# Kernel optimization log

Hardware: AMD Instinct MI355X
Metric: run time of the kernel (lower is better)

## Reference

```python
import jax, jax.numpy as jnp
import numpy as np

WINDOW_SIZE = 11
CHANNEL = 3
PAD = WINDOW_SIZE // 2
C1 = 0.01 ** 2
C2 = 0.03 ** 2
LEVEL_WEIGHTS = np.array([0.0448, 0.2856, 0.3001, 0.2363, 0.1333], dtype=np.float32)


def _make_window():
    # 1D Gaussian, sigma=1.5, normalized; outer product -> 2D window
    x = np.arange(WINDOW_SIZE, dtype=np.float32)
    g = np.exp(-((x - WINDOW_SIZE // 2) ** 2) / (2.0 * 1.5 ** 2))
    g = g / g.sum()
    w2 = np.outer(g, g).astype(np.float32)  # [11,11]
    # depthwise kernel [C, 1, 11, 11]
    return jnp.asarray(np.tile(w2[None, None], (CHANNEL, 1, 1, 1)))


def setup_inputs() -> dict:
    key = jax.random.key(0)
    k1, k2 = jax.random.split(key)
    img1 = jax.random.uniform(k1, (16, 3, 512, 512), dtype=jnp.float32)
    # correlated second image so cs stays positive (cs**weight well-defined)
    img2 = jnp.clip(img1 + 0.05 * jax.random.normal(k2, img1.shape, dtype=jnp.float32), 0.0, 1.0)
    return {"img1": img1, "img2": img2, "window": _make_window()}


def _dwconv(x, window):
    # depthwise 11x11 conv, SAME padding (pad=5), groups=C
    return jax.lax.conv_general_dilated(
        x, window, window_strides=(1, 1), padding=[(PAD, PAD), (PAD, PAD)],
        feature_group_count=CHANNEL,
        dimension_numbers=("NCHW", "OIHW", "NCHW"))


def _ssim_and_cs(img1, img2, window):
    mu1 = _dwconv(img1, window)
    mu2 = _dwconv(img2, window)
    mu1_sq = mu1 * mu1
    mu2_sq = mu2 * mu2
    mu1_mu2 = mu1 * mu2
    sigma1_sq = _dwconv(img1 * img1, window) - mu1_sq
    sigma2_sq = _dwconv(img2 * img2, window) - mu2_sq
    sigma12 = _dwconv(img1 * img2, window) - mu1_mu2
    cs_map = (2.0 * sigma12 + C2) / (sigma1_sq + sigma2_sq + C2)
    ssim_map = (2.0 * mu1_mu2 + C1) / (mu1_sq + mu2_sq + C1) * cs_map
    return jnp.mean(ssim_map), jnp.mean(cs_map)


def _avg_pool2(x):
    B, C, H, W = x.shape
    return x.reshape(B, C, H // 2, 2, W // 2, 2).mean(axis=(3, 5))


def reference(img1, img2, window):
    weights = jnp.asarray(LEVEL_WEIGHTS)
    levels = weights.shape[0]
    mssim, mcs = [], []
    for i in range(levels):
        s, c = _ssim_and_cs(img1, img2, window)
        mssim.append(s)
        mcs.append(c)
        if i < levels - 1:
            img1 = _avg_pool2(img1)
            img2 = _avg_pool2(img2)
    mssim = jnp.stack(mssim)
    mcs = jnp.stack(mcs)
    return jnp.prod(mcs[:-1] ** weights[:-1]) * mssim[-1] ** weights[-1]
```

## Files before the change

### kernel.cpp

```cpp
#include <hip/hip_runtime.h>
#include <math.h>

#define TW 16
#define THT 64
#define HRT 74
#define SS 66
#define HS 64
#define SC1 0.0001f
#define SC2 0.0009f
#define PLANES 48
#define NSLOT 64

typedef float v2f __attribute__((ext_vector_type(2)));

struct alignas(16) Smem {
    float sb[HRT * SS];
    float hb[HRT * HS];
    float rbuf[8];
};

__device__ __forceinline__ void ssim_tile(
        Smem* sm,
        const float* __restrict__ p1, const float* __restrict__ p2,
        int H, int W, int tx, int ty, int level,
        const float* __restrict__ window,
        float* __restrict__ accum,
        float* __restrict__ l1a, float* __restrict__ l1b,
        float* __restrict__ l2a, float* __restrict__ l2b,
        float* __restrict__ l3a, float* __restrict__ l3b,
        float* __restrict__ l4a, float* __restrict__ l4b)
{
    const int tid = threadIdx.x;
    float* sb = sm->sb;
    float* hb = sm->hb;

    float g[11];
    {
        float invg5 = 1.0f / sqrtf(window[60]);
        #pragma unroll
        for (int k = 0; k < 11; ++k) g[k] = window[55 + k] * invg5;
    }

    const bool interior = (ty >= 5) && (ty + HRT - 6 < H) &&
                          (tx >= 8) && (tx + 24 <= W);
    if (interior) {
        for (int s = tid; s < HRT * 8; s += 256) {
            int r = s >> 3, j = s & 7;
            size_t o = (size_t)(ty + r - 5) * W + (tx - 8 + 4 * j);
            float4 a = *(const float4*)(p1 + o);
            float4 b = *(const float4*)(p2 + o);
            float* d = &sb[SS * r + 8 * j];
            *(float2*)(d)     = make_float2(a.x + b.x, a.x - b.x);
            *(float2*)(d + 2) = make_float2(a.y + b.y, a.y - b.y);
            *(float2*)(d + 4) = make_float2(a.z + b.z, a.z - b.z);
            *(float2*)(d + 6) = make_float2(a.w + b.w, a.w - b.w);
        }
    } else {
        for (int s = tid; s < HRT * 16; s += 256) {
            int r = s >> 4, j = s & 15;
            int gy = ty + r - 5;
            int gx = tx - 8 + 2 * j;
            float2 v1 = make_float2(0.f, 0.f), v2 = make_float2(0.f, 0.f);
            if ((unsigned)gy < (unsigned)H && (unsigned)gx < (unsigned)W) {
                size_t o = (size_t)gy * W + gx;
                v1 = *(const float2*)(p1 + o);
                v2 = *(const float2*)(p2 + o);
            }
            float* d = &sb[SS * r + 4 * j];
            *(float2*)(d)     = make_float2(v1.x + v2.x, v1.x - v2.x);
            *(float2*)(d + 2) = make_float2(v1.y + v2.y, v1.y - v2.y);
        }
    }
    __syncthreads();

    if (l1a) {
        int pc = tid & 7;
        int pr = tid >> 3;
        int r  = 2 * pr + 5;
        int x0 = 2 * (2 * pc + 8);
        const v2f* r0p = (const v2f*)&sb[SS * r + x0];
        const v2f* r1p = (const v2f*)&sb[SS * (r + 1) + x0];
        v2f s = (r0p[0] + r0p[1]) + (r1p[0] + r1p[1]);
        int W2 = W >> 1;
        size_t o = (size_t)((ty >> 1) + pr) * W2 + (tx >> 1) + pc;
        l1a[o] = 0.125f * (s.x + s.y);
        l1b[o] = 0.125f * (s.x - s.y);
    }

    if (l1a && tid >= 192) {
        const int lane = tid - 192;
        int qr = lane >> 2, qc = lane & 3;
        int rb = 4 * qr + 5, cb = 4 * qc + 8;
        v2f acc = {0.f, 0.f};
        #pragma unroll
        for (int i = 0; i < 4; ++i) {
            int ii = (i + qc) & 3;
            #pragma unroll
            for (int j = 0; j < 4; ++j) {
                int jr = (j + qr) & 3;
                acc += *(const v2f*)&sb[SS * (rb + ii) + 2 * (cb + jr)];
            }
        }
        float v2a = 0.03125f * (acc.x + acc.y), v2b = 0.03125f * (acc.x - acc.y);
        {
            int W4 = W >> 2;
            size_t o = (size_t)((ty >> 2) + qr) * W4 + (tx >> 2) + qc;
            l2a[o] = v2a;
            l2b[o] = v2b;
        }
        float v3a, v3b;
        {
            int tr = (lane >> 1) & 7, tc = lane & 1;
            int l00 = 8 * tr + 2 * tc;
            v3a = 0.25f * (__shfl(v2a, l00) + __shfl(v2a, l00 + 1) +
                           __shfl(v2a, l00 + 4) + __shfl(v2a, l00 + 5));
            v3b = 0.25f * (__shfl(v2b, l00) + __shfl(v2b, l00 + 1) +
                           __shfl(v2b, l00 + 4) + __shfl(v2b, l00 + 5));
            if (lane < 16) {
                int W8 = W >> 3;
                size_t o = (size_t)((ty >> 3) + tr) * W8 + (tx >> 3) + tc;
                l3a[o] = v3a;
                l3b[o] = v3b;
            }
        }
        {
            int ur = lane & 3;
            float v4a = 0.25f * (__shfl(v3a, 4 * ur) + __shfl(v3a, 4 * ur + 1) +
                                 __shfl(v3a, 4 * ur + 2) + __shfl(v3a, 4 * ur + 3));
            float v4b = 0.25f * (__shfl(v3b, 4 * ur) + __shfl(v3b, 4 * ur + 1) +
                                 __shfl(v3b, 4 * ur + 2) + __shfl(v3b, 4 * ur + 3));
            if (lane < 4) {
                int W16 = W >> 4;
                size_t o = (size_t)((ty >> 4) + ur) * W16 + (tx >> 4);
                l4a[o] = v4a;
                l4b[o] = v4b;
            }
        }
    }

    for (int gi = tid; gi < HRT * 8; gi += 256) {
        int r  = gi >> 3;
        int c0 = (gi & 7) << 1;
        const v2f* src = (const v2f*)&sb[SS * r + 2 * (c0 + 3)];
        v2f am_a = {0,0}, aq_a = {0,0};
        v2f am_b = {0,0}, aq_b = {0,0};
        #pragma unroll
        for (int k = 0; k < 12; ++k) {
            v2f uv = src[k];
            v2f sq = uv * uv;
            if (k < 11) {
                v2f gg = {g[k], g[k]};
                am_a += gg * uv;
                aq_a += gg * sq;
            }
            if (k >= 1) {
                v2f gg = {g[k - 1], g[k - 1]};
                am_b += gg * uv;
                aq_b += gg * sq;
            }
        }
        int rx = (r & 1) << 2;
        *(float4*)&hb[HS * r + ((4 * c0)     ^ rx)] = make_float4(am_a.x, am_a.y, aq_a.x, aq_a.y);
        *(float4*)&hb[HS * r + ((4 * c0 + 4) ^ rx)] = make_float4(am_b.x, am_b.y, aq_b.x, aq_b.y);
    }
    __syncthreads();

    float ssum = 0.f, csum = 0.f;
    {
        int c  = tid & 15;
        int r0 = (tid >> 4) << 2;
        v2f M[4] = {{0,0},{0,0},{0,0},{0,0}};
        v2f Q[4] = {{0,0},{0,0},{0,0},{0,0}};
        #pragma unroll
        for (int k = 0; k < 14; ++k) {
            int R = r0 + k;
            float4 h = *(const float4*)&hb[HS * R + ((4 * c) ^ ((R & 1) << 2))];
            v2f hm = {h.x, h.y};
            v2f hq = {h.z, h.w};
            #pragma unroll
            for (int j = 0; j < 4; ++j) {
                int t = k - j;
                if (t >= 0 && t < 11) {
                    v2f gg = {g[t], g[t]};
                    M[j] += gg * hm;
                    Q[j] += gg * hq;
                }
            }
        }
        #pragma unroll
        for (int j = 0; j < 4; ++j) {
            if (ty + r0 + j < H) {
                float P = M[j].x * M[j].x, Qm = M[j].y * M[j].y;
                float A = 0.5f * (P - Qm);
                float B = 0.5f * (P + Qm);
                float su = 0.5f * (Q[j].x + Q[j].y);
                float sd = 0.5f * (Q[j].x - Q[j].y);
                float n1 = A + SC1;
                float d1 = B + SC1;
                float n2 = sd - A + SC2;
                float d2 = su - B + SC2;
                float inv = 1.f / (d1 * d2);
                csum += n2 * d1 * inv;
                ssum += n1 * n2 * inv;
            }
        }
    }

    #pragma unroll
    for (int off = 32; off; off >>= 1) {
        ssum += __shfl_down(ssum, off);
        csum += __shfl_down(csum, off);
    }
    const int wid = tid >> 6, lane = tid & 63;
    if (lane == 0) { sm->rbuf[wid * 2] = ssum; sm->rbuf[wid * 2 + 1] = csum; }
    __syncthreads();
    if (tid == 0) {
        float S = sm->rbuf[0] + sm->rbuf[2] + sm->rbuf[4] + sm->rbuf[6];
        float C = sm->rbuf[1] + sm->rbuf[3] + sm->rbuf[5] + sm->rbuf[7];
        int slot = (blockIdx.x + blockIdx.y * 7 + blockIdx.z * 13) & (NSLOT - 1);
        atomicAdd(&accum[(2 * level) * NSLOT + slot], S);
        atomicAdd(&accum[(2 * level + 1) * NSLOT + slot], C);
    }
}

__global__ __launch_bounds__(256, 4) void ssim_l0(
        const float* __restrict__ img1, const float* __restrict__ img2,
        const float* __restrict__ window, float* __restrict__ accum,
        float* __restrict__ l1a, float* __restrict__ l1b,
        float* __restrict__ l2a, float* __restrict__ l2b,
        float* __restrict__ l3a, float* __restrict__ l3b,
        float* __restrict__ l4a, float* __restrict__ l4b)
{
    __shared__ Smem sm;
    const int lin = blockIdx.x + (blockIdx.y << 5) + (blockIdx.z << 8);
    const int swz = (lin & 7) * 1536 + (lin >> 3);
    const int plane = swz >> 8;
    const int rem   = swz & 255;
    const int tyi   = rem >> 5;
    const int txi   = rem & 31;
    ssim_tile(&sm,
              img1 + (size_t)plane * 512 * 512,
              img2 + (size_t)plane * 512 * 512,
              512, 512, txi * TW, tyi * THT, 0,
              window, accum,
              l1a + (size_t)plane * 256 * 256, l1b + (size_t)plane * 256 * 256,
              l2a + (size_t)plane * 128 * 128, l2b + (size_t)plane * 128 * 128,
              l3a + (size_t)plane * 64 * 64,   l3b + (size_t)plane * 64 * 64,
              l4a + (size_t)plane * 32 * 32,   l4b + (size_t)plane * 32 * 32);
}

__global__ __launch_bounds__(256, 4) void ssim_rest(
        const float* __restrict__ l1a, const float* __restrict__ l1b,
        const float* __restrict__ l2a, const float* __restrict__ l2b,
        const float* __restrict__ l3a, const float* __restrict__ l3b,
        const float* __restrict__ l4a, const float* __restrict__ l4b,
        const float* __restrict__ window, float* __restrict__ accum)
{
    __shared__ Smem sm;
    const int x = blockIdx.x;
    const int plane = blockIdx.z;
    int level, H, tix, tiy;
    const float *b1, *b2;
    if (x < 64)      { level = 1; H = 256; tix = x & 15;           tiy = x >> 4;      b1 = l1a; b2 = l1b; }
    else if (x < 80) { level = 2; H = 128; int i = x - 64; tix = i & 7; tiy = i >> 3; b1 = l2a; b2 = l2b; }
    else if (x < 84) { level = 3; H = 64;  int i = x - 80; tix = i;     tiy = 0;      b1 = l3a; b2 = l3b; }
    else             { level = 4; H = 32;  int i = x - 84; tix = i;     tiy = 0;      b1 = l4a; b2 = l4b; }
    const float* p1 = b1 + (size_t)plane * H * H;
    const float* p2 = b2 + (size_t)plane * H * H;
    ssim_tile(&sm, p1, p2, H, H, tix * TW, tiy * THT, level,
              window, accum,
              nullptr, nullptr, nullptr, nullptr,
              nullptr, nullptr, nullptr, nullptr);
}

__global__ void finalize_kernel(const float* __restrict__ accum, float* __restrict__ out) {
    int t = threadIdx.x;
    float sums[10];
    #pragma unroll
    for (int i = 0; i < 10; ++i) {
        float v = accum[i * NSLOT + t];
        #pragma unroll
        for (int off = 32; off; off >>= 1) v += __shfl_down(v, off);
        sums[i] = v;
    }
    if (t == 0) {
        const float w[5] = {0.0448f, 0.2856f, 0.3001f, 0.2363f, 0.1333f};
        float res = 1.f;
        #pragma unroll
        for (int L = 0; L < 4; ++L) {
            float dim = (float)(512 >> L);
            float cnt = (float)PLANES * dim * dim;
            res *= powf(sums[2 * L + 1] / cnt, w[L]);
        }
        float cnt4 = (float)PLANES * 32.f * 32.f;
        res *= powf(sums[8] / cnt4, w[4]);
        out[0] = res;
    }
}

extern "C" void kernel_launch(void* const* d_in, const int* in_sizes, int n_in,
                              void* d_out, int out_size, void* d_ws, size_t ws_size,
                              hipStream_t stream) {
    const float* img1   = (const float*)d_in[0];
    const float* img2   = (const float*)d_in[1];
    const float* window = (const float*)d_in[2];
    float* out = (float*)d_out;
    float* ws  = (float*)d_ws;

    float* accum = ws;
    const size_t S1 = (size_t)PLANES * 256 * 256;
    const size_t S2 = (size_t)PLANES * 128 * 128;
    const size_t S3 = (size_t)PLANES * 64 * 64;
    const size_t S4 = (size_t)PLANES * 32 * 32;
    float* l1a = ws + 1024;    float* l1b = l1a + S1;
    float* l2a = l1b + S1;     float* l2b = l2a + S2;
    float* l3a = l2b + S2;     float* l3b = l3a + S3;
    float* l4a = l3b + S3;     float* l4b = l4a + S4;

    hipMemsetAsync(accum, 0, 10 * NSLOT * sizeof(float), stream);

    ssim_l0<<<dim3(512 / TW, 512 / THT, PLANES), 256, 0, stream>>>(
        img1, img2, window, accum,
        l1a, l1b, l2a, l2b, l3a, l3b, l4a, l4b);

    ssim_rest<<<dim3(86, 1, PLANES), 256, 0, stream>>>(
        l1a, l1b, l2a, l2b, l3a, l3b, l4a, l4b, window, accum);

    finalize_kernel<<<1, 64, 0, stream>>>(accum, out);
}
```

Before: 219.4 us.

## Widen horizontal blur per thread, split level-1 kernel, trim small-level halo rows

The horizontal Gaussian pass now produces four output columns per thread instead of two, so each loaded shared-memory pair is reused across more taps and fewer threads do the row loop. Level 1 gets its own kernel with a swizzled block order, and levels 2-4 run in a separate launch. That launch clamps the halo row count to the image height so it skips staging and filtering rows beyond the image. A template flag removes the row bounds check for full-size tiles. The trade-offs are higher register pressure in the horizontal pass and one extra kernel launch.

```diff
diff --git a/kernel.cpp b/kernel.cpp
--- a/kernel.cpp
+++ b/kernel.cpp
@@ -19,10 +19,11 @@
     float rbuf[8];
 };
 
+template<bool GUARD>
 __device__ __forceinline__ void ssim_tile(
         Smem* sm,
         const float* __restrict__ p1, const float* __restrict__ p2,
-        int H, int W, int tx, int ty, int level,
+        int H, int W, int tx, int ty, int hrt, int level,
         const float* __restrict__ window,
         float* __restrict__ accum,
         float* __restrict__ l1a, float* __restrict__ l1b,
@@ -56,7 +57,7 @@
             *(float2*)(d + 6) = make_float2(a.w + b.w, a.w - b.w);
         }
     } else {
-        for (int s = tid; s < HRT * 16; s += 256) {
+        for (int s = tid; s < hrt * 16; s += 256) {
             int r = s >> 4, j = s & 15;
             int gy = ty + r - 5;
             int gx = tx - 8 + 2 * j;
@@ -138,30 +139,31 @@
         }
     }
 
-    for (int gi = tid; gi < HRT * 8; gi += 256) {
-        int r  = gi >> 3;
-        int c0 = (gi & 7) << 1;
+    for (int gi = tid; gi < hrt * 4; gi += 256) {
+        int r  = gi >> 2;
+        int c0 = (gi & 3) << 2;
         const v2f* src = (const v2f*)&sb[SS * r + 2 * (c0 + 3)];
-        v2f am_a = {0,0}, aq_a = {0,0};
-        v2f am_b = {0,0}, aq_b = {0,0};
-        #pragma unroll
-        for (int k = 0; k < 12; ++k) {
+        v2f am[4] = {{0,0},{0,0},{0,0},{0,0}};
+        v2f aq[4] = {{0,0},{0,0},{0,0},{0,0}};
+        #pragma unroll
+        for (int k = 0; k < 14; ++k) {
             v2f uv = src[k];
             v2f sq = uv * uv;
-            if (k < 11) {
-                v2f gg = {g[k], g[k]};
-                am_a += gg * uv;
-                aq_a += gg * sq;
-            }
-            if (k >= 1) {
-                v2f gg = {g[k - 1], g[k - 1]};
-                am_b += gg * uv;
-                aq_b += gg * sq;
+            #pragma unroll
+            for (int q = 0; q < 4; ++q) {
+                int t = k - q;
+                if (t >= 0 && t < 11) {
+                    v2f gg = {g[t], g[t]};
+                    am[q] += gg * uv;
+                    aq[q] += gg * sq;
+                }
             }
         }
         int rx = (r & 1) << 2;
-        *(float4*)&hb[HS * r + ((4 * c0)     ^ rx)] = make_float4(am_a.x, am_a.y, aq_a.x, aq_a.y);
-        *(float4*)&hb[HS * r + ((4 * c0 + 4) ^ rx)] = make_float4(am_b.x, am_b.y, aq_b.x, aq_b.y);
+        #pragma unroll
+        for (int q = 0; q < 4; ++q)
+            *(float4*)&hb[HS * r + ((4 * (c0 + q)) ^ rx)] =
+                make_float4(am[q].x, am[q].y, aq[q].x, aq[q].y);
     }
     __syncthreads();
 
@@ -189,7 +191,7 @@
         }
         #pragma unroll
         for (int j = 0; j < 4; ++j) {
-            if (ty + r0 + j < H) {
+            if (!GUARD || (ty + r0 + j < H)) {
                 float P = M[j].x * M[j].x, Qm = M[j].y * M[j].y;
                 float A = 0.5f * (P - Qm);
                 float B = 0.5f * (P + Qm);
@@ -238,10 +240,10 @@
     const int rem   = swz & 255;
     const int tyi   = rem >> 5;
     const int txi   = rem & 31;
-    ssim_tile(&sm,
+    ssim_tile<false>(&sm,
               img1 + (size_t)plane * 512 * 512,
               img2 + (size_t)plane * 512 * 512,
-              512, 512, txi * TW, tyi * THT, 0,
+              512, 512, txi * TW, tyi * THT, HRT, 0,
               window, accum,
               l1a + (size_t)plane * 256 * 256, l1b + (size_t)plane * 256 * 256,
               l2a + (size_t)plane * 128 * 128, l2b + (size_t)plane * 128 * 128,
@@ -249,8 +251,26 @@
               l4a + (size_t)plane * 32 * 32,   l4b + (size_t)plane * 32 * 32);
 }
 
-__global__ __launch_bounds__(256, 4) void ssim_rest(
+__global__ __launch_bounds__(256, 4) void ssim_l1(
         const float* __restrict__ l1a, const float* __restrict__ l1b,
+        const float* __restrict__ window, float* __restrict__ accum)
+{
+    __shared__ Smem sm;
+    const int lin = blockIdx.x + (blockIdx.z << 6);
+    const int swz = (lin & 7) * 384 + (lin >> 3);
+    const int plane = swz >> 6;
+    const int rem   = swz & 63;
+    const int tiy   = rem >> 4;
+    const int tix   = rem & 15;
+    const float* p1 = l1a + (size_t)plane * 256 * 256;
+    const float* p2 = l1b + (size_t)plane * 256 * 256;
+    ssim_tile<false>(&sm, p1, p2, 256, 256, tix * TW, tiy * THT, HRT, 1,
+              window, accum,
+              nullptr, nullptr, nullptr, nullptr,
+              nullptr, nullptr, nullptr, nullptr);
+}
+
+__global__ __launch_bounds__(256, 4) void ssim_l234(
         const float* __restrict__ l2a, const float* __restrict__ l2b,
         const float* __restrict__ l3a, const float* __restrict__ l3b,
         const float* __restrict__ l4a, const float* __restrict__ l4b,
@@ -261,13 +281,14 @@
     const int plane = blockIdx.z;
     int level, H, tix, tiy;
     const float *b1, *b2;
-    if (x < 64)      { level = 1; H = 256; tix = x & 15;           tiy = x >> 4;      b1 = l1a; b2 = l1b; }
-    else if (x < 80) { level = 2; H = 128; int i = x - 64; tix = i & 7; tiy = i >> 3; b1 = l2a; b2 = l2b; }
-    else if (x < 84) { level = 3; H = 64;  int i = x - 80; tix = i;     tiy = 0;      b1 = l3a; b2 = l3b; }
-    else             { level = 4; H = 32;  int i = x - 84; tix = i;     tiy = 0;      b1 = l4a; b2 = l4b; }
+    if (x < 16)      { level = 2; H = 128; tix = x & 7;  tiy = x >> 3; b1 = l2a; b2 = l2b; }
+    else if (x < 20) { level = 3; H = 64;  tix = x - 16; tiy = 0;      b1 = l3a; b2 = l3b; }
+    else             { level = 4; H = 32;  tix = x - 20; tiy = 0;      b1 = l4a; b2 = l4b; }
     const float* p1 = b1 + (size_t)plane * H * H;
     const float* p2 = b2 + (size_t)plane * H * H;
-    ssim_tile(&sm, p1, p2, H, H, tix * TW, tiy * THT, level,
+    int ty = tiy * THT;
+    int hrt = min(HRT, H - ty + 10);
+    ssim_tile<true>(&sm, p1, p2, H, H, tix * TW, ty, hrt, level,
               window, accum,
               nullptr, nullptr, nullptr, nullptr,
               nullptr, nullptr, nullptr, nullptr);
@@ -323,8 +344,10 @@
         img1, img2, window, accum,
         l1a, l1b, l2a, l2b, l3a, l3b, l4a, l4b);
 
-    ssim_rest<<<dim3(86, 1, PLANES), 256, 0, stream>>>(
-        l1a, l1b, l2a, l2b, l3a, l3b, l4a, l4b, window, accum);
+    ssim_l1<<<dim3(64, 1, PLANES), 256, 0, stream>>>(l1a, l1b, window, accum);
+
+    ssim_l234<<<dim3(22, 1, PLANES), 256, 0, stream>>>(
+        l2a, l2b, l3a, l3b, l4a, l4b, window, accum);
 
     finalize_kernel<<<1, 64, 0, stream>>>(accum, out);
 }
```

New measurement: 223.9 us. 1.02x slower.
